# Kernel tuning notes

Measured on AMD Instinct MI355X. Metric: run time of the kernel, lower is better.

Reference implementation:

```python
import jax, jax.numpy as jnp
import numpy as np

B, P, N, M = 8, 50, 128, 128          # batch, pomo, query nodes, route tokens
EMB, H, D = 128, 8, 16                # embedding_dim, head_num, qkv_dim
NE, K = 8, 2                          # num_experts, top-k
CLIP = 10.0                           # logit_clipping


def setup_inputs() -> dict:
    key = jax.random.key(0)
    ks = jax.random.split(key, 12)
    s = 0.02
    return {
        "encoded_nodes": jax.random.normal(ks[0], (B, P, N, EMB), jnp.float32),
        "encoded_routes": jax.random.normal(ks[1], (B, P, M, EMB + 1), jnp.float32),
        "ninf_mask": jnp.zeros((B, P, N), jnp.float32),
        "route_mask": jnp.zeros((B, P, N, M), jnp.float32),
        "Wq": s * jax.random.normal(ks[2], (EMB, H * D), jnp.float32),
        "Wk": s * jax.random.normal(ks[3], (EMB + 1, H * D), jnp.float32),
        "Wv": s * jax.random.normal(ks[4], (EMB + 1, H * D), jnp.float32),
        "Wg": s * jax.random.normal(ks[5], (H * D, NE), jnp.float32),
        "We": s * jax.random.normal(ks[6], (NE, H * D, EMB + 1), jnp.float32),
        "be": jnp.zeros((NE, EMB + 1), jnp.float32),
        "Wfinal": s * jax.random.normal(ks[7], (EMB + 1, 1), jnp.float32),
    }


def _heads(x, W):
    # x: [B,P,n,F] @ W[F,H*D] -> [B,P,H,n,D]
    y = x @ W
    b, p, n, _ = y.shape
    return jnp.swapaxes(y.reshape(b, p, n, H, D), 2, 3)


def reference(encoded_nodes, encoded_routes, ninf_mask, route_mask,
              Wq, Wk, Wv, Wg, We, be, Wfinal):
    # --- masked multi-head attention (multi_head_attention1) ---
    q = _heads(encoded_nodes, Wq)          # [B,P,H,N,D]
    k = _heads(encoded_routes, Wk)         # [B,P,H,M,D]
    v = _heads(encoded_routes, Wv)         # [B,P,H,M,D]
    score = jnp.einsum('bphnd,bphmd->bphnm', q, k) / jnp.sqrt(jnp.float32(D))
    score = score + route_mask[:, :, None, :, :]          # rank3 ninf mask
    w = jax.nn.softmax(score, axis=-1)
    # rank2 mask applied multiplicatively after softmax
    keep = jnp.where(ninf_mask == 0.0, 1.0, 0.0)[:, :, None, :, None]
    w = w * keep
    out = jnp.einsum('bphnm,bphmd->bphnd', w, v)
    out_concat = jnp.swapaxes(out, 2, 3).reshape(B, P, N, H * D)

    # --- top-k gated MoE combine (noisy gating, eval: no noise) ---
    x = out_concat.reshape(-1, H * D)                     # [T, H*D]
    T = x.shape[0]
    gate_logits = x @ Wg                                  # [T, NE]
    top_vals, top_idx = jax.lax.top_k(gate_logits, K)
    top_g = jax.nn.softmax(top_vals, axis=-1)
    gates = jnp.zeros((T, NE), x.dtype).at[jnp.arange(T)[:, None], top_idx].set(top_g)
    expert_out = jnp.einsum('ti,eio->teo', x, We) + be    # [T, NE, EMB+1]
    moe_out = jnp.einsum('te,teo->to', gates, expert_out)
    importance = gates.sum(0)
    moe_loss = importance.var() / (importance.mean() ** 2 + 1e-10)
    mh_atten_out = moe_out.reshape(B, P, N, EMB + 1)

    # --- final scoring ---
    score_scaled = (mh_atten_out @ Wfinal)[..., 0]        # [B,P,N]
    score_clipped = CLIP * jnp.tanh(score_scaled)
    score_masked = score_clipped + ninf_mask
    probs = jax.nn.softmax(score_masked, axis=2)
    return probs, moe_loss
```

## Files before the change

### kernel.cpp

```cpp
#include <hip/hip_runtime.h>

constexpr int B  = 8,  P = 50, N = 128, M = 128;
constexpr int EMB = 128, H = 8, D = 16;
constexpr int NE = 8;
constexpr int HD = H * D;
constexpr int E1 = EMB + 1;
constexpr int BP = B * P;
constexpr int T  = BP * N;

__global__ void prep_kernel(const float* __restrict__ We,
                            const float* __restrict__ be,
                            const float* __restrict__ Wf,
                            float* __restrict__ Wep, float* __restrict__ bpv,
                            float* __restrict__ importance) {
    const int e = blockIdx.x;
    const int f = threadIdx.x;

    float a = 0.f;
    const long base = ((long)e * HD + f) * E1;
    for (int o = 0; o < E1; ++o) a += We[base + o] * Wf[o];
    Wep[e * HD + f] = a;

    if (f == 0) {
        float b = 0.f;
        for (int o = 0; o < E1; ++o) b += be[(long)e * E1 + o] * Wf[o];
        bpv[e] = b;
    }
    if (e == 0 && f < NE) importance[f] = 0.f;
}

__global__ __launch_bounds__(128) void proj_kernel(
    const float* __restrict__ nodes,
    const float* __restrict__ routes,
    const float* __restrict__ Wq, const float* __restrict__ Wk,
    const float* __restrict__ Wv,
    float* __restrict__ qo, float* __restrict__ ko, float* __restrict__ vo) {
    const int mat = blockIdx.y;
    const float* __restrict__ X = (mat == 0) ? nodes : routes;
    const float* __restrict__ W = (mat == 0) ? Wq : (mat == 1 ? Wk : Wv);
    float* __restrict__ out     = (mat == 0) ? qo : (mat == 1 ? ko : vo);
    const int Kd = (mat == 0) ? EMB : E1;

    const int row0 = blockIdx.x * 64;
    const int tid  = threadIdx.x;
    const int tr   = tid >> 4;
    const int tc   = tid & 15;

    __shared__ float XT[8][68];
    __shared__ float WS[8][132];

    float acc[8][8];
    #pragma unroll
    for (int i = 0; i < 8; ++i)
        #pragma unroll
        for (int j = 0; j < 8; ++j) acc[i][j] = 0.f;

    for (int kk = 0; kk < Kd; kk += 8) {
        const int kw = (Kd - kk) < 8 ? (Kd - kk) : 8;
        #pragma unroll
        for (int i = 0; i < 4; ++i) {
            int e = tid + i * 128;
            int kx = e & 7, r = e >> 3;
            XT[kx][r] = (kx < kw) ? X[(long)(row0 + r) * Kd + kk + kx] : 0.f;
        }
        #pragma unroll
        for (int i = 0; i < 2; ++i) {
            int e  = tid + i * 128;
            int kx = e >> 5, c4 = (e & 31) * 4;
            float4 w4 = make_float4(0.f, 0.f, 0.f, 0.f);
            if (kx < kw) w4 = *(const float4*)&W[(long)(kk + kx) * HD + c4];
            *(float4*)&WS[kx][c4] = w4;
        }
        __syncthreads();

        #pragma unroll
        for (int k = 0; k < 8; ++k) {
            float4 xa = *(const float4*)&XT[k][tr * 4];
            float4 xb = *(const float4*)&XT[k][32 + tr * 4];
            float4 wa = *(const float4*)&WS[k][tc * 4];
            float4 wb = *(const float4*)&WS[k][64 + tc * 4];
            float xr[8] = {xa.x, xa.y, xa.z, xa.w, xb.x, xb.y, xb.z, xb.w};
            float wc[8] = {wa.x, wa.y, wa.z, wa.w, wb.x, wb.y, wb.z, wb.w};
            #pragma unroll
            for (int i = 0; i < 8; ++i)
                #pragma unroll
                for (int j = 0; j < 8; ++j) acc[i][j] += xr[i] * wc[j];
        }
        __syncthreads();
    }

    #pragma unroll
    for (int ig = 0; ig < 2; ++ig)
        #pragma unroll
        for (int i = 0; i < 4; ++i) {
            int r = row0 + ig * 32 + tr * 4 + i;
            float4 o0 = make_float4(acc[ig*4+i][0], acc[ig*4+i][1],
                                    acc[ig*4+i][2], acc[ig*4+i][3]);
            float4 o1 = make_float4(acc[ig*4+i][4], acc[ig*4+i][5],
                                    acc[ig*4+i][6], acc[ig*4+i][7]);
            *(float4*)&out[(long)r * HD + tc * 4]      = o0;
            *(float4*)&out[(long)r * HD + 64 + tc * 4] = o1;
        }
}

__global__ __launch_bounds__(64) void attn_kernel(
    const float* __restrict__ qbuf,
    const float* __restrict__ kbuf,
    const float* __restrict__ vbuf,
    const float* __restrict__ rmask,
    const float* __restrict__ ninf,
    float* __restrict__ xcat) {
    const int bp  = blockIdx.x;
    const int h   = blockIdx.y;
    const int tid = threadIdx.x;

    const long t0 = (long)bp * N + tid, t1 = t0 + 64;

    float qr0[16], qr1[16];
    {
        const float4* q0 = (const float4*)&qbuf[t0 * HD + h * D];
        const float4* q1 = (const float4*)&qbuf[t1 * HD + h * D];
        #pragma unroll
        for (int i = 0; i < 4; ++i) {
            float4 a = q0[i], b = q1[i];
            qr0[i*4+0] = a.x*0.25f; qr0[i*4+1] = a.y*0.25f;
            qr0[i*4+2] = a.z*0.25f; qr0[i*4+3] = a.w*0.25f;
            qr1[i*4+0] = b.x*0.25f; qr1[i*4+1] = b.y*0.25f;
            qr1[i*4+2] = b.z*0.25f; qr1[i*4+3] = b.w*0.25f;
        }
    }

    const float* __restrict__ kbase = kbuf + ((long)bp * M) * HD + h * D;
    const float* __restrict__ vbase = vbuf + ((long)bp * M) * HD + h * D;
    const float4* rm0 = (const float4*)&rmask[t0 * M];
    const float4* rm1 = (const float4*)&rmask[t1 * M];

    float sum0 = 0.f, sum1 = 0.f;
    float o0[16], o1[16];
    #pragma unroll
    for (int d = 0; d < 16; ++d) { o0[d] = 0.f; o1[d] = 0.f; }

    for (int mb = 0; mb < 32; ++mb) {
        float4 r0 = rm0[mb], r1 = rm1[mb];
        float r0v[4] = {r0.x, r0.y, r0.z, r0.w};
        float r1v[4] = {r1.x, r1.y, r1.z, r1.w};
        #pragma unroll
        for (int j = 0; j < 4; ++j) {
            const int m = mb * 4 + j;
            const float4* k4 = (const float4*)&kbase[(long)m * HD];
            const float4* v4 = (const float4*)&vbase[(long)m * HD];
            float s0 = 0.f, s1 = 0.f;
            #pragma unroll
            for (int q4 = 0; q4 < 4; ++q4) {
                float4 kq = k4[q4];
                s0 += qr0[q4*4+0]*kq.x + qr0[q4*4+1]*kq.y
                    + qr0[q4*4+2]*kq.z + qr0[q4*4+3]*kq.w;
                s1 += qr1[q4*4+0]*kq.x + qr1[q4*4+1]*kq.y
                    + qr1[q4*4+2]*kq.z + qr1[q4*4+3]*kq.w;
            }
            float e0 = __expf(s0 + r0v[j]);
            float e1 = __expf(s1 + r1v[j]);
            sum0 += e0; sum1 += e1;
            #pragma unroll
            for (int q4 = 0; q4 < 4; ++q4) {
                float4 vq = v4[q4];
                o0[q4*4+0] += e0*vq.x; o0[q4*4+1] += e0*vq.y;
                o0[q4*4+2] += e0*vq.z; o0[q4*4+3] += e0*vq.w;
                o1[q4*4+0] += e1*vq.x; o1[q4*4+1] += e1*vq.y;
                o1[q4*4+2] += e1*vq.z; o1[q4*4+3] += e1*vq.w;
            }
        }
    }

    const float inv0 = ((ninf[t0] == 0.f) ? 1.f : 0.f) / sum0;
    const float inv1 = ((ninf[t1] == 0.f) ? 1.f : 0.f) / sum1;
    #pragma unroll
    for (int q4 = 0; q4 < 4; ++q4) {
        float4 w0 = make_float4(o0[q4*4+0]*inv0, o0[q4*4+1]*inv0,
                                o0[q4*4+2]*inv0, o0[q4*4+3]*inv0);
        float4 w1 = make_float4(o1[q4*4+0]*inv1, o1[q4*4+1]*inv1,
                                o1[q4*4+2]*inv1, o1[q4*4+3]*inv1);
        *(float4*)&xcat[t0 * HD + h * D + q4 * 4] = w0;
        *(float4*)&xcat[t1 * HD + h * D + q4 * 4] = w1;
    }
}

__global__ __launch_bounds__(128) void moe_final_kernel(
    const float* __restrict__ xcat, const float* __restrict__ Wg,
    const float* __restrict__ ninf, const float* __restrict__ Wep,
    const float* __restrict__ bpv, float* __restrict__ importance,
    float* __restrict__ out) {
    __shared__ float WgS[EMB][NE];
    __shared__ float WeS[NE][132];
    __shared__ float red[N];
    __shared__ float impS[NE];

    const int bp = blockIdx.x;
    const int n  = threadIdx.x;

    #pragma unroll
    for (int i = 0; i < 2; ++i) {
        int e = n + i * 128;
        int r = e >> 1, c4 = (e & 1) * 4;
        *(float4*)&WgS[r][c4] = *(const float4*)&Wg[(long)r * NE + c4];
    }
    #pragma unroll
    for (int i = 0; i < 2; ++i) {
        int idx = n + i * 128;
        int r = idx >> 5, c = (idx & 31) * 4;
        *(float4*)&WeS[r][c] = *(const float4*)&Wep[(long)r * HD + c];
    }
    if (n < NE) impS[n] = 0.f;
    __syncthreads();

    const long t = (long)bp * N + n;
    const float4* row4 = (const float4*)&xcat[t * HD];

    float gl[NE];
    #pragma unroll
    for (int e = 0; e < NE; ++e) gl[e] = 0.f;
    for (int fb = 0; fb < 32; ++fb) {
        float4 xv = row4[fb];
        float x4[4] = {xv.x, xv.y, xv.z, xv.w};
        #pragma unroll
        for (int j = 0; j < 4; ++j)
            #pragma unroll
            for (int e = 0; e < NE; ++e) gl[e] += x4[j] * WgS[fb * 4 + j][e];
    }

    int e0 = 0; float v0 = gl[0];
    #pragma unroll
    for (int e = 1; e < NE; ++e) if (gl[e] > v0) { v0 = gl[e]; e0 = e; }
    int e1 = -1; float v1 = -3.4e38f;
    #pragma unroll
    for (int e = 0; e < NE; ++e) if (e != e0 && gl[e] > v1) { v1 = gl[e]; e1 = e; }
    float ex = __expf(v1 - v0);
    float g0 = 1.f / (1.f + ex);
    float g1 = ex / (1.f + ex);

    atomicAdd(&impS[e0], g0);
    atomicAdd(&impS[e1], g1);

    float s = g0 * bpv[e0] + g1 * bpv[e1];
    for (int fb = 0; fb < 32; ++fb) {
        float4 xv = row4[fb];
        float x4[4] = {xv.x, xv.y, xv.z, xv.w};
        #pragma unroll
        for (int j = 0; j < 4; ++j) {
            int f = fb * 4 + j;
            s += x4[j] * (g0 * WeS[e0][f] + g1 * WeS[e1][f]);
        }
    }
    s = 10.f * tanhf(s) + ninf[t];

    red[n] = s;
    __syncthreads();
    for (int off = 64; off > 0; off >>= 1) {
        if (n < off) red[n] = fmaxf(red[n], red[n + off]);
        __syncthreads();
    }
    float mx = red[0];
    __syncthreads();
    float e = __expf(s - mx);
    red[n] = e;
    __syncthreads();
    for (int off = 64; off > 0; off >>= 1) {
        if (n < off) red[n] += red[n + off];
        __syncthreads();
    }
    float sum = red[0];

    out[t] = e / sum;

    if (n < NE) atomicAdd(&importance[n], impS[n]);
}

__global__ void loss_kernel(const float* __restrict__ importance,
                            float* __restrict__ out) {
    if (threadIdx.x == 0) {
        float mean = 0.f;
        #pragma unroll
        for (int e = 0; e < NE; ++e) mean += importance[e];
        mean *= (1.f / NE);
        float var = 0.f;
        #pragma unroll
        for (int e = 0; e < NE; ++e) {
            float d = importance[e] - mean;
            var += d * d;
        }
        var *= (1.f / NE);
        out[T] = var / (mean * mean + 1e-10f);
    }
}

extern "C" void kernel_launch(void* const* d_in, const int* in_sizes, int n_in,
                              void* d_out, int out_size, void* d_ws, size_t ws_size,
                              hipStream_t stream) {
    const float* nodes  = (const float*)d_in[0];
    const float* routes = (const float*)d_in[1];
    const float* ninf   = (const float*)d_in[2];
    const float* rmask  = (const float*)d_in[3];
    const float* Wq     = (const float*)d_in[4];
    const float* Wk     = (const float*)d_in[5];
    const float* Wv     = (const float*)d_in[6];
    const float* Wg     = (const float*)d_in[7];
    const float* We     = (const float*)d_in[8];
    const float* be     = (const float*)d_in[9];
    const float* Wfin   = (const float*)d_in[10];

    float* ws = (float*)d_ws;
    float* Wep        = ws + 16;
    float* bpv        = ws + 1040;
    float* importance = ws + 1048;
    float* qbuf       = ws + 4096;
    float* kbuf       = qbuf + (long)T * HD;
    float* vbuf       = kbuf + (long)T * HD;
    float* xcat       = vbuf + (long)T * HD;

    float* out = (float*)d_out;

    prep_kernel<<<NE, 128, 0, stream>>>(We, be, Wfin, Wep, bpv, importance);
    proj_kernel<<<dim3(800, 3), 128, 0, stream>>>(nodes, routes, Wq, Wk, Wv,
                                                  qbuf, kbuf, vbuf);
    attn_kernel<<<dim3(BP, H), 64, 0, stream>>>(qbuf, kbuf, vbuf,
                                                rmask, ninf, xcat);
    moe_final_kernel<<<BP, 128, 0, stream>>>(xcat, Wg, ninf, Wep, bpv,
                                             importance, out);
    loss_kernel<<<1, 64, 0, stream>>>(importance, out);
}
```

Baseline: 307.8 us.

## Double-buffer projection GEMM, widen attention per-thread rows, split MoE rows across thread pairs

The projection GEMM now uses 256-thread blocks over 128-row tiles and double-buffers its shared-memory tiles with register prefetch, overlapping global loads with compute. The attention kernel packs two heads per 64-thread block and has each thread process four query rows, so every K/V load is reused across more rows at the cost of higher register pressure. The MoE/final kernel gives each token two threads that split the gate and expert dot products and combine them with shuffles. Together these aim to improve load reuse and latency hiding, though fewer attention blocks and heavier register use could lower occupancy.

```diff
diff --git a/kernel.cpp b/kernel.cpp
--- a/kernel.cpp
+++ b/kernel.cpp
@@ -29,7 +29,7 @@
     if (e == 0 && f < NE) importance[f] = 0.f;
 }
 
-__global__ __launch_bounds__(128) void proj_kernel(
+__global__ __launch_bounds__(256) void proj_kernel(
     const float* __restrict__ nodes,
     const float* __restrict__ routes,
     const float* __restrict__ Wq, const float* __restrict__ Wk,
@@ -40,14 +40,15 @@
     const float* __restrict__ W = (mat == 0) ? Wq : (mat == 1 ? Wk : Wv);
     float* __restrict__ out     = (mat == 0) ? qo : (mat == 1 ? ko : vo);
     const int Kd = (mat == 0) ? EMB : E1;
-
-    const int row0 = blockIdx.x * 64;
+    const int nit = (Kd + 7) >> 3;
+
+    const int row0 = blockIdx.x * 128;
     const int tid  = threadIdx.x;
     const int tr   = tid >> 4;
     const int tc   = tid & 15;
 
-    __shared__ float XT[8][68];
-    __shared__ float WS[8][132];
+    __shared__ float XT[2][8][132];
+    __shared__ float WS[2][8][132];
 
     float acc[8][8];
     #pragma unroll
@@ -55,52 +56,70 @@
         #pragma unroll
         for (int j = 0; j < 8; ++j) acc[i][j] = 0.f;
 
-    for (int kk = 0; kk < Kd; kk += 8) {
-        const int kw = (Kd - kk) < 8 ? (Kd - kk) : 8;
+    float xr[4];
+    float4 wr;
+    const int xkx = tid & 7, xrr = tid >> 3;
+    const int wkx = tid >> 5, wc4 = (tid & 31) * 4;
+
+    {
         #pragma unroll
         for (int i = 0; i < 4; ++i) {
-            int e = tid + i * 128;
-            int kx = e & 7, r = e >> 3;
-            XT[kx][r] = (kx < kw) ? X[(long)(row0 + r) * Kd + kk + kx] : 0.f;
-        }
-        #pragma unroll
-        for (int i = 0; i < 2; ++i) {
-            int e  = tid + i * 128;
-            int kx = e >> 5, c4 = (e & 31) * 4;
-            float4 w4 = make_float4(0.f, 0.f, 0.f, 0.f);
-            if (kx < kw) w4 = *(const float4*)&W[(long)(kk + kx) * HD + c4];
-            *(float4*)&WS[kx][c4] = w4;
-        }
-        __syncthreads();
+            int kg = xkx;
+            xr[i] = (kg < Kd) ? X[(long)(row0 + xrr + i * 32) * Kd + kg] : 0.f;
+        }
+        wr = (wkx < Kd) ? *(const float4*)&W[(long)wkx * HD + wc4]
+                        : make_float4(0.f, 0.f, 0.f, 0.f);
+        #pragma unroll
+        for (int i = 0; i < 4; ++i) XT[0][xkx][xrr + i * 32] = xr[i];
+        *(float4*)&WS[0][wkx][wc4] = wr;
+    }
+    __syncthreads();
+
+    for (int it = 0; it < nit; ++it) {
+        const int buf = it & 1;
+        if (it + 1 < nit) {
+            const int kk = (it + 1) * 8;
+            #pragma unroll
+            for (int i = 0; i < 4; ++i) {
+                int kg = kk + xkx;
+                xr[i] = (kg < Kd) ? X[(long)(row0 + xrr + i * 32) * Kd + kg] : 0.f;
+            }
+            int kg = kk + wkx;
+            wr = (kg < Kd) ? *(const float4*)&W[(long)kg * HD + wc4]
+                           : make_float4(0.f, 0.f, 0.f, 0.f);
+        }
 
         #pragma unroll
         for (int k = 0; k < 8; ++k) {
-            float4 xa = *(const float4*)&XT[k][tr * 4];
-            float4 xb = *(const float4*)&XT[k][32 + tr * 4];
-            float4 wa = *(const float4*)&WS[k][tc * 4];
-            float4 wb = *(const float4*)&WS[k][64 + tc * 4];
-            float xr[8] = {xa.x, xa.y, xa.z, xa.w, xb.x, xb.y, xb.z, xb.w};
-            float wc[8] = {wa.x, wa.y, wa.z, wa.w, wb.x, wb.y, wb.z, wb.w};
+            float4 xa = *(const float4*)&XT[buf][k][tr * 4];
+            float4 xb = *(const float4*)&XT[buf][k][64 + tr * 4];
+            float4 wa = *(const float4*)&WS[buf][k][tc * 4];
+            float4 wb = *(const float4*)&WS[buf][k][64 + tc * 4];
+            float xv[8] = {xa.x, xa.y, xa.z, xa.w, xb.x, xb.y, xb.z, xb.w};
+            float wv[8] = {wa.x, wa.y, wa.z, wa.w, wb.x, wb.y, wb.z, wb.w};
             #pragma unroll
             for (int i = 0; i < 8; ++i)
                 #pragma unroll
-                for (int j = 0; j < 8; ++j) acc[i][j] += xr[i] * wc[j];
+                for (int j = 0; j < 8; ++j) acc[i][j] += xv[i] * wv[j];
+        }
+
+        if (it + 1 < nit) {
+            const int nb = buf ^ 1;
+            #pragma unroll
+            for (int i = 0; i < 4; ++i) XT[nb][xkx][xrr + i * 32] = xr[i];
+            *(float4*)&WS[nb][wkx][wc4] = wr;
         }
         __syncthreads();
     }
 
     #pragma unroll
-    for (int ig = 0; ig < 2; ++ig)
-        #pragma unroll
-        for (int i = 0; i < 4; ++i) {
-            int r = row0 + ig * 32 + tr * 4 + i;
-            float4 o0 = make_float4(acc[ig*4+i][0], acc[ig*4+i][1],
-                                    acc[ig*4+i][2], acc[ig*4+i][3]);
-            float4 o1 = make_float4(acc[ig*4+i][4], acc[ig*4+i][5],
-                                    acc[ig*4+i][6], acc[ig*4+i][7]);
-            *(float4*)&out[(long)r * HD + tc * 4]      = o0;
-            *(float4*)&out[(long)r * HD + 64 + tc * 4] = o1;
-        }
+    for (int i = 0; i < 8; ++i) {
+        int r = row0 + (i < 4 ? 0 : 64) + tr * 4 + (i & 3);
+        float4 o0 = make_float4(acc[i][0], acc[i][1], acc[i][2], acc[i][3]);
+        float4 o1 = make_float4(acc[i][4], acc[i][5], acc[i][6], acc[i][7]);
+        *(float4*)&out[(long)r * HD + tc * 4]      = o0;
+        *(float4*)&out[(long)r * HD + 64 + tc * 4] = o1;
+    }
 }
 
 __global__ __launch_bounds__(64) void attn_kernel(
@@ -110,82 +129,91 @@
     const float* __restrict__ rmask,
     const float* __restrict__ ninf,
     float* __restrict__ xcat) {
-    const int bp  = blockIdx.x;
-    const int h   = blockIdx.y;
-    const int tid = threadIdx.x;
-
-    const long t0 = (long)bp * N + tid, t1 = t0 + 64;
-
-    float qr0[16], qr1[16];
-    {
-        const float4* q0 = (const float4*)&qbuf[t0 * HD + h * D];
-        const float4* q1 = (const float4*)&qbuf[t1 * HD + h * D];
-        #pragma unroll
-        for (int i = 0; i < 4; ++i) {
-            float4 a = q0[i], b = q1[i];
-            qr0[i*4+0] = a.x*0.25f; qr0[i*4+1] = a.y*0.25f;
-            qr0[i*4+2] = a.z*0.25f; qr0[i*4+3] = a.w*0.25f;
-            qr1[i*4+0] = b.x*0.25f; qr1[i*4+1] = b.y*0.25f;
-            qr1[i*4+2] = b.z*0.25f; qr1[i*4+3] = b.w*0.25f;
+    const int bp   = blockIdx.x;
+    const int h    = blockIdx.y * 2 + (threadIdx.x >> 5);
+    const int lane = threadIdx.x & 31;
+
+    long t[4];
+    #pragma unroll
+    for (int i = 0; i < 4; ++i) t[i] = (long)bp * N + lane + i * 32;
+
+    float qr[4][16];
+    #pragma unroll
+    for (int i = 0; i < 4; ++i) {
+        const float4* q4 = (const float4*)&qbuf[t[i] * HD + h * D];
+        #pragma unroll
+        for (int c = 0; c < 4; ++c) {
+            float4 a = q4[c];
+            qr[i][c*4+0] = a.x * 0.25f; qr[i][c*4+1] = a.y * 0.25f;
+            qr[i][c*4+2] = a.z * 0.25f; qr[i][c*4+3] = a.w * 0.25f;
         }
     }
 
     const float* __restrict__ kbase = kbuf + ((long)bp * M) * HD + h * D;
     const float* __restrict__ vbase = vbuf + ((long)bp * M) * HD + h * D;
-    const float4* rm0 = (const float4*)&rmask[t0 * M];
-    const float4* rm1 = (const float4*)&rmask[t1 * M];
-
-    float sum0 = 0.f, sum1 = 0.f;
-    float o0[16], o1[16];
-    #pragma unroll
-    for (int d = 0; d < 16; ++d) { o0[d] = 0.f; o1[d] = 0.f; }
+    const float4* rm[4];
+    #pragma unroll
+    for (int i = 0; i < 4; ++i) rm[i] = (const float4*)&rmask[t[i] * M];
+
+    float sum[4] = {0.f, 0.f, 0.f, 0.f};
+    float o[4][16];
+    #pragma unroll
+    for (int i = 0; i < 4; ++i)
+        #pragma unroll
+        for (int d = 0; d < 16; ++d) o[i][d] = 0.f;
 
     for (int mb = 0; mb < 32; ++mb) {
-        float4 r0 = rm0[mb], r1 = rm1[mb];
-        float r0v[4] = {r0.x, r0.y, r0.z, r0.w};
-        float r1v[4] = {r1.x, r1.y, r1.z, r1.w};
+        float4 r4[4];
+        #pragma unroll
+        for (int i = 0; i < 4; ++i) r4[i] = rm[i][mb];
         #pragma unroll
         for (int j = 0; j < 4; ++j) {
             const int m = mb * 4 + j;
             const float4* k4 = (const float4*)&kbase[(long)m * HD];
             const float4* v4 = (const float4*)&vbase[(long)m * HD];
-            float s0 = 0.f, s1 = 0.f;
-            #pragma unroll
-            for (int q4 = 0; q4 < 4; ++q4) {
-                float4 kq = k4[q4];
-                s0 += qr0[q4*4+0]*kq.x + qr0[q4*4+1]*kq.y
-                    + qr0[q4*4+2]*kq.z + qr0[q4*4+3]*kq.w;
-                s1 += qr1[q4*4+0]*kq.x + qr1[q4*4+1]*kq.y
-                    + qr1[q4*4+2]*kq.z + qr1[q4*4+3]*kq.w;
+            float kq[16];
+            #pragma unroll
+            for (int c = 0; c < 4; ++c) {
+                float4 kk = k4[c];
+                kq[c*4+0] = kk.x; kq[c*4+1] = kk.y;
+                kq[c*4+2] = kk.z; kq[c*4+3] = kk.w;
             }
-            float e0 = __expf(s0 + r0v[j]);
-            float e1 = __expf(s1 + r1v[j]);
-            sum0 += e0; sum1 += e1;
-            #pragma unroll
-            for (int q4 = 0; q4 < 4; ++q4) {
-                float4 vq = v4[q4];
-                o0[q4*4+0] += e0*vq.x; o0[q4*4+1] += e0*vq.y;
-                o0[q4*4+2] += e0*vq.z; o0[q4*4+3] += e0*vq.w;
-                o1[q4*4+0] += e1*vq.x; o1[q4*4+1] += e1*vq.y;
-                o1[q4*4+2] += e1*vq.z; o1[q4*4+3] += e1*vq.w;
+            float e[4];
+            #pragma unroll
+            for (int i = 0; i < 4; ++i) {
+                float s = 0.f;
+                #pragma unroll
+                for (int d = 0; d < 16; ++d) s += qr[i][d] * kq[d];
+                float rmv = (j == 0) ? r4[i].x : (j == 1) ? r4[i].y
+                           : (j == 2) ? r4[i].z : r4[i].w;
+                e[i] = __expf(s + rmv);
+                sum[i] += e[i];
             }
-        }
-    }
-
-    const float inv0 = ((ninf[t0] == 0.f) ? 1.f : 0.f) / sum0;
-    const float inv1 = ((ninf[t1] == 0.f) ? 1.f : 0.f) / sum1;
-    #pragma unroll
-    for (int q4 = 0; q4 < 4; ++q4) {
-        float4 w0 = make_float4(o0[q4*4+0]*inv0, o0[q4*4+1]*inv0,
-                                o0[q4*4+2]*inv0, o0[q4*4+3]*inv0);
-        float4 w1 = make_float4(o1[q4*4+0]*inv1, o1[q4*4+1]*inv1,
-                                o1[q4*4+2]*inv1, o1[q4*4+3]*inv1);
-        *(float4*)&xcat[t0 * HD + h * D + q4 * 4] = w0;
-        *(float4*)&xcat[t1 * HD + h * D + q4 * 4] = w1;
-    }
-}
-
-__global__ __launch_bounds__(128) void moe_final_kernel(
+            #pragma unroll
+            for (int c = 0; c < 4; ++c) {
+                float4 vv = v4[c];
+                #pragma unroll
+                for (int i = 0; i < 4; ++i) {
+                    o[i][c*4+0] += e[i] * vv.x; o[i][c*4+1] += e[i] * vv.y;
+                    o[i][c*4+2] += e[i] * vv.z; o[i][c*4+3] += e[i] * vv.w;
+                }
+            }
+        }
+    }
+
+    #pragma unroll
+    for (int i = 0; i < 4; ++i) {
+        const float inv = ((ninf[t[i]] == 0.f) ? 1.f : 0.f) / sum[i];
+        #pragma unroll
+        for (int c = 0; c < 4; ++c) {
+            float4 w = make_float4(o[i][c*4+0]*inv, o[i][c*4+1]*inv,
+                                   o[i][c*4+2]*inv, o[i][c*4+3]*inv);
+            *(float4*)&xcat[t[i] * HD + h * D + c * 4] = w;
+        }
+    }
+}
+
+__global__ __launch_bounds__(256) void moe_final_kernel(
     const float* __restrict__ xcat, const float* __restrict__ Wg,
     const float* __restrict__ ninf, const float* __restrict__ Wep,
     const float* __restrict__ bpv, float* __restrict__ importance,
@@ -195,37 +223,41 @@
     __shared__ float red[N];
     __shared__ float impS[NE];
 
-    const int bp = blockIdx.x;
-    const int n  = threadIdx.x;
-
-    #pragma unroll
-    for (int i = 0; i < 2; ++i) {
-        int e = n + i * 128;
-        int r = e >> 1, c4 = (e & 1) * 4;
+    const int bp   = blockIdx.x;
+    const int tid  = threadIdx.x;
+    const int n    = tid >> 1;
+    const int half = tid & 1;
+
+    {
+        int r = tid >> 1, c4 = (tid & 1) * 4;
         *(float4*)&WgS[r][c4] = *(const float4*)&Wg[(long)r * NE + c4];
     }
-    #pragma unroll
-    for (int i = 0; i < 2; ++i) {
-        int idx = n + i * 128;
-        int r = idx >> 5, c = (idx & 31) * 4;
+    {
+        int r = tid >> 5, c = (tid & 31) * 4;
         *(float4*)&WeS[r][c] = *(const float4*)&Wep[(long)r * HD + c];
     }
-    if (n < NE) impS[n] = 0.f;
+    if (tid < NE) impS[tid] = 0.f;
     __syncthreads();
 
     const long t = (long)bp * N + n;
     const float4* row4 = (const float4*)&xcat[t * HD];
 
-    float gl[NE];
-    #pragma unroll
-    for (int e = 0; e < NE; ++e) gl[e] = 0.f;
+    const int eb = half * 4;
+    float glp[4] = {0.f, 0.f, 0.f, 0.f};
     for (int fb = 0; fb < 32; ++fb) {
         float4 xv = row4[fb];
         float x4[4] = {xv.x, xv.y, xv.z, xv.w};
         #pragma unroll
         for (int j = 0; j < 4; ++j)
             #pragma unroll
-            for (int e = 0; e < NE; ++e) gl[e] += x4[j] * WgS[fb * 4 + j][e];
+            for (int e = 0; e < 4; ++e) glp[e] += x4[j] * WgS[fb * 4 + j][eb + e];
+    }
+    float gl[NE];
+    #pragma unroll
+    for (int e = 0; e < 4; ++e) {
+        float other = __shfl_xor(glp[e], 1);
+        gl[0 + e] = half ? other : glp[e];
+        gl[4 + e] = half ? glp[e] : other;
     }
 
     int e0 = 0; float v0 = gl[0];
@@ -238,41 +270,45 @@
     float g0 = 1.f / (1.f + ex);
     float g1 = ex / (1.f + ex);
 
-    atomicAdd(&impS[e0], g0);
-    atomicAdd(&impS[e1], g1);
-
-    float s = g0 * bpv[e0] + g1 * bpv[e1];
-    for (int fb = 0; fb < 32; ++fb) {
+    if (half == 0) {
+        atomicAdd(&impS[e0], g0);
+        atomicAdd(&impS[e1], g1);
+    }
+
+    float sp = 0.f;
+    for (int fb = half * 16; fb < half * 16 + 16; ++fb) {
         float4 xv = row4[fb];
         float x4[4] = {xv.x, xv.y, xv.z, xv.w};
         #pragma unroll
         for (int j = 0; j < 4; ++j) {
             int f = fb * 4 + j;
-            s += x4[j] * (g0 * WeS[e0][f] + g1 * WeS[e1][f]);
-        }
-    }
+            sp += x4[j] * (g0 * WeS[e0][f] + g1 * WeS[e1][f]);
+        }
+    }
+    float spo = __shfl_xor(sp, 1);
+    float lo = half ? spo : sp, hi = half ? sp : spo;
+    float s = (g0 * bpv[e0] + g1 * bpv[e1]) + lo + hi;
     s = 10.f * tanhf(s) + ninf[t];
 
-    red[n] = s;
+    if (half == 0) red[n] = s;
     __syncthreads();
     for (int off = 64; off > 0; off >>= 1) {
-        if (n < off) red[n] = fmaxf(red[n], red[n + off]);
+        if (tid < off) red[tid] = fmaxf(red[tid], red[tid + off]);
         __syncthreads();
     }
     float mx = red[0];
     __syncthreads();
     float e = __expf(s - mx);
-    red[n] = e;
+    if (half == 0) red[n] = e;
     __syncthreads();
     for (int off = 64; off > 0; off >>= 1) {
-        if (n < off) red[n] += red[n + off];
+        if (tid < off) red[tid] += red[tid + off];
         __syncthreads();
     }
     float sum = red[0];
 
-    out[t] = e / sum;
-
-    if (n < NE) atomicAdd(&importance[n], impS[n]);
+    if (half == 0) out[t] = e / sum;
+    if (tid < NE) atomicAdd(&importance[tid], impS[tid]);
 }
 
 __global__ void loss_kernel(const float* __restrict__ importance,
@@ -320,11 +356,11 @@
     float* out = (float*)d_out;
 
     prep_kernel<<<NE, 128, 0, stream>>>(We, be, Wfin, Wep, bpv, importance);
-    proj_kernel<<<dim3(800, 3), 128, 0, stream>>>(nodes, routes, Wq, Wk, Wv,
+    proj_kernel<<<dim3(400, 3), 256, 0, stream>>>(nodes, routes, Wq, Wk, Wv,
                                                   qbuf, kbuf, vbuf);
-    attn_kernel<<<dim3(BP, H), 64, 0, stream>>>(qbuf, kbuf, vbuf,
+    attn_kernel<<<dim3(BP, 4), 64, 0, stream>>>(qbuf, kbuf, vbuf,
                                                 rmask, ninf, xcat);
-    moe_final_kernel<<<BP, 128, 0, stream>>>(xcat, Wg, ninf, Wep, bpv,
+    moe_final_kernel<<<BP, 256, 0, stream>>>(xcat, Wg, ninf, Wep, bpv,
                                              importance, out);
     loss_kernel<<<1, 64, 0, stream>>>(importance, out);
 }
```

After: 437.1 us. 1.42x slower.
